# Kernel optimization log

Hardware: AMD Instinct MI355X
Metric: run time of the kernel (lower is better)

The kernel has to match this reference:

```python
import jax, jax.numpy as jnp
import numpy as np

N = 32768      # nodes
E = 524288     # edges (avg degree 16)
F = 64         # node_feat_dim
D = 64         # gnn_dim (= per-head out channels, concat=False)
ED = 32        # edge_feat_dim
L = 6          # num_layers
H = 2          # heads
C = D          # per-head channels
LN_EPS = 1e-5


def layer_norm(h, g, b):
    mu = jnp.mean(h, axis=-1, keepdims=True)
    var = jnp.mean((h - mu) ** 2, axis=-1, keepdims=True)
    return g * (h - mu) * jax.lax.rsqrt(var + LN_EPS) + b


def setup_inputs() -> dict:
    key = jax.random.key(0)
    ks = jax.random.split(key, 16)
    x = jax.random.normal(ks[0], (N, F), jnp.float32)
    edge_index = jax.random.randint(ks[1], (2, E), 0, N, jnp.int32)
    edge_attr = jax.random.normal(ks[2], (E, ED), jnp.float32)
    manual_gamma = 1.0 + 0.1 * jax.random.normal(ks[3], (L, D), jnp.float32)
    manual_beta = 0.1 * jax.random.normal(ks[4], (L, D), jnp.float32)
    # node_embed Linear(F, D)
    embed_W = jax.random.normal(ks[5], (F, D), jnp.float32) / np.float32(np.sqrt(F))
    embed_b = jnp.zeros((D,), jnp.float32)
    # per-layer LayerNorm affine params
    ln_gamma = jnp.ones((L, D), jnp.float32)
    ln_beta = jnp.zeros((L, D), jnp.float32)
    # per-layer GATConv params (shared lin for src/dst, PyG non-bipartite)
    lin_W = jax.random.normal(ks[6], (L, D, H * C), jnp.float32) / np.float32(np.sqrt(D))
    lin_edge_W = jax.random.normal(ks[7], (L, ED, H * C), jnp.float32) / np.float32(np.sqrt(ED))
    att_src = jax.random.normal(ks[8], (L, H, C), jnp.float32) / np.float32(np.sqrt(C))
    att_dst = jax.random.normal(ks[9], (L, H, C), jnp.float32) / np.float32(np.sqrt(C))
    att_edge = jax.random.normal(ks[10], (L, H, C), jnp.float32) / np.float32(np.sqrt(C))
    gat_bias = jnp.zeros((L, C), jnp.float32)
    # edge output head: Linear(2D+ED, D) -> ReLU -> Linear(D, 1)
    head_W1 = jax.random.normal(ks[11], (2 * D + ED, D), jnp.float32) / np.float32(np.sqrt(2 * D + ED))
    head_b1 = jnp.zeros((D,), jnp.float32)
    head_W2 = jax.random.normal(ks[12], (D, 1), jnp.float32) / np.float32(np.sqrt(D))
    head_b2 = jnp.zeros((1,), jnp.float32)
    return dict(x=x, edge_index=edge_index, edge_attr=edge_attr,
                manual_gamma=manual_gamma, manual_beta=manual_beta,
                embed_W=embed_W, embed_b=embed_b, ln_gamma=ln_gamma, ln_beta=ln_beta,
                lin_W=lin_W, lin_edge_W=lin_edge_W, att_src=att_src, att_dst=att_dst,
                att_edge=att_edge, gat_bias=gat_bias, head_W1=head_W1, head_b1=head_b1,
                head_W2=head_W2, head_b2=head_b2)


def reference(x, edge_index, edge_attr, manual_gamma, manual_beta,
              embed_W, embed_b, ln_gamma, ln_beta, lin_W, lin_edge_W,
              att_src, att_dst, att_edge, gat_bias, head_W1, head_b1,
              head_W2, head_b2):
    src, dst = edge_index[0], edge_index[1]
    # PyG GATConv default add_self_loops=True, fill_value='mean' for edge_attr
    loop = jnp.arange(N, dtype=edge_index.dtype)
    src_f = jnp.concatenate([src, loop])   # [E+N]
    dst_f = jnp.concatenate([dst, loop])
    deg = jax.ops.segment_sum(jnp.ones((E,), x.dtype), dst, num_segments=N)
    loop_attr = jax.ops.segment_sum(edge_attr, dst, num_segments=N) / jnp.maximum(deg, 1.0)[:, None]
    edge_attr_f = jnp.concatenate([edge_attr, loop_attr], axis=0)  # [E+N, ED]

    h = x @ embed_W + embed_b  # [N, D]
    for l in range(L):
        hn = layer_norm(h, ln_gamma[l], ln_beta[l])
        hm = manual_gamma[l][None, :] * hn + manual_beta[l][None, :]
        xh = (hm @ lin_W[l]).reshape(N, H, C)                      # [N,H,C]
        a_s = jnp.sum(xh * att_src[l][None], axis=-1)              # [N,H]
        a_d = jnp.sum(xh * att_dst[l][None], axis=-1)              # [N,H]
        eh = (edge_attr_f @ lin_edge_W[l]).reshape(-1, H, C)       # [E+N,H,C]
        a_e = jnp.sum(eh * att_edge[l][None], axis=-1)             # [E+N,H]
        alpha = jax.nn.leaky_relu(a_s[src_f] + a_d[dst_f] + a_e, 0.2)
        amax = jax.ops.segment_max(alpha, dst_f, num_segments=N)   # every node has a self-loop
        ex = jnp.exp(alpha - amax[dst_f])
        den = jax.ops.segment_sum(ex, dst_f, num_segments=N)
        w = ex / (den[dst_f] + 1e-16)                              # segment softmax [E+N,H]
        msg = xh[src_f] * w[..., None]                             # [E+N,H,C]
        out = jax.ops.segment_sum(msg, dst_f, num_segments=N)      # [N,H,C]
        h = jax.nn.relu(jnp.mean(out, axis=1) + gat_bias[l])       # concat=False -> head mean

    ef = jnp.concatenate([h[src], h[dst], edge_attr], axis=-1)     # [E, 2D+ED]
    hid = jax.nn.relu(ef @ head_W1 + head_b1)
    return (hid @ head_W2 + head_b2)[:, 0]                         # [E]
```

## Files before the change

### kernel.cpp

```cpp
#include <hip/hip_runtime.h>
#include <hip/hip_bf16.h>
#include <math.h>

#define NN 32768
#define EE 524288
#define LL 6

typedef __attribute__((ext_vector_type(8))) short short8;
typedef __attribute__((ext_vector_type(4))) float floatx4;
typedef __attribute__((ext_vector_type(4))) float fx4;
typedef __attribute__((ext_vector_type(2))) float fx2;

union U16x8 { short8 v; unsigned short u[8]; };

__device__ __forceinline__ unsigned short f2bf(float x) {
    union { float f; unsigned int u; } v; v.f = x;
    unsigned int r = v.u + 0x7fffu + ((v.u >> 16) & 1u);
    return (unsigned short)(r >> 16);
}
__device__ __forceinline__ float bf2f(unsigned short h) {
    union { unsigned int u; float f; } v; v.u = (unsigned int)h << 16;
    return v.f;
}


__global__ void deg_kernel(const int* __restrict__ dst, int* __restrict__ deg) {
    int i = (blockIdx.x * 256 + threadIdx.x) * 4;
    int4 d = *(const int4*)(dst + i);
    atomicAdd(&deg[d.x], 1);
    atomicAdd(&deg[d.y], 1);
    atomicAdd(&deg[d.z], 1);
    atomicAdd(&deg[d.w], 1);
}

__global__ __launch_bounds__(1024) void scan_kernel(const int* __restrict__ deg,
                                                    int* __restrict__ row_ptr,
                                                    int* __restrict__ cnt) {
    __shared__ int bs[1024];
    int t = threadIdx.x;
    int base = t * 32;
    int loc[32];
    int s = 0;
#pragma unroll
    for (int i = 0; i < 32; ++i) { int v = deg[base + i]; loc[i] = s; s += v; }
    bs[t] = s;
    __syncthreads();
    for (int off = 1; off < 1024; off <<= 1) {
        int v = (t >= off) ? bs[t - off] : 0;
        __syncthreads();
        bs[t] += v;
        __syncthreads();
    }
    int pre = (t == 0) ? 0 : bs[t - 1];
#pragma unroll
    for (int i = 0; i < 32; ++i) { row_ptr[base + i] = pre + loc[i]; cnt[base + i] = 0; }
    if (t == 1023) row_ptr[NN] = bs[1023];
}

__global__ void fill_kernel(const int* __restrict__ src, const int* __restrict__ dst,
                            const int* __restrict__ row_ptr, int* __restrict__ cnt,
                            int2* __restrict__ sedge) {
    int e = blockIdx.x * 256 + threadIdx.x;
    if (e >= EE) return;
    int d = dst[e];
    int pos = row_ptr[d] + atomicAdd(&cnt[d], 1);
    sedge[pos] = make_int2(e, src[e]);
}

__global__ __launch_bounds__(256) void smallprep_kernel(
    const float* __restrict__ lin_W, const float* __restrict__ head_W1,
    const float* __restrict__ lin_edge_W, const float* __restrict__ att_edge,
    const float* __restrict__ att_src, const float* __restrict__ att_dst,
    unsigned short* __restrict__ gBhi, unsigned short* __restrict__ gBlo,
    unsigned short* __restrict__ aeBhi, unsigned short* __restrict__ aeBlo,
    float* __restrict__ vs, float* __restrict__ vvd,
    unsigned short* __restrict__ w1chi, unsigned short* __restrict__ w1clo,
    int* __restrict__ deg) {
    __shared__ float svb[384];
    int bb = blockIdx.x;
    int tid = threadIdx.x;
    if (bb < 7) {
        unsigned short* dh = gBhi + (size_t)bb * 128 * 64;
        unsigned short* dl = gBlo + (size_t)bb * 128 * 64;
        if (bb < 6) {
            int n2 = tid & 63, kh = tid >> 6;
            U16x8 hh[4], ll[4];
            for (int kk = 0; kk < 32; ++kk) {
                int j = kh * 32 + kk;
                int h = j >> 6, k = j & 63;
                float wv = 0.5f * lin_W[((size_t)bb * 64 + k) * 128 + h * 64 + n2];
                unsigned short h16 = f2bf(wv);
                hh[kk >> 3].u[kk & 7] = h16;
                ll[kk >> 3].u[kk & 7] = f2bf(wv - bf2f(h16));
            }
#pragma unroll
            for (int c = 0; c < 4; ++c) {
                int cg = kh * 4 + c;
                int off = n2 * 128 + ((cg ^ (n2 & 15)) << 3);
                *(short8*)(dh + off) = hh[c].v;
                *(short8*)(dl + off) = ll[c].v;
            }
        } else {
            int n = tid & 127, kh = tid >> 7;
            U16x8 hh[4], ll[4];
            for (int kk = 0; kk < 32; ++kk) {
                int k = kh * 32 + kk;
                float wv = (n < 64) ? head_W1[k * 64 + n] : head_W1[(64 + k) * 64 + (n - 64)];
                unsigned short h16 = f2bf(wv);
                hh[kk >> 3].u[kk & 7] = h16;
                ll[kk >> 3].u[kk & 7] = f2bf(wv - bf2f(h16));
            }
#pragma unroll
            for (int c = 0; c < 4; ++c) {
                int cg = kh * 4 + c;
                int off = n * 64 + ((cg ^ (n & 7)) << 3);
                *(short8*)(dh + off) = hh[c].v;
                *(short8*)(dl + off) = ll[c].v;
            }
        }
    } else if (bb == 7) {
        for (int t = tid; t < 384; t += 256) {
            int l = t / 64; int r = t & 63; int ed = r >> 1; int hh = r & 1;
            const float* w = lin_edge_W + l * 32 * 128 + ed * 128 + hh * 64;
            const float* a = att_edge + l * 128 + hh * 64;
            float s = 0.f;
#pragma unroll 8
            for (int c = 0; c < 64; ++c) s += w[c] * a[c];
            svb[t] = s;
        }
        int n = tid & 63, kc = tid >> 6;
#pragma unroll
        for (int j = 0; j < 8; ++j) {
            int k = kc * 8 + j;
            float wv = head_W1[(128 + k) * 64 + n];
            unsigned short h16 = f2bf(wv);
            w1chi[n * 32 + k] = h16;
            w1clo[n * 32 + k] = f2bf(wv - bf2f(h16));
        }
        __syncthreads();
        if (tid < 64) {
            int n2 = tid & 15, q = tid >> 4;
            U16x8 hi, lo;
#pragma unroll
            for (int i = 0; i < 8; ++i) {
                int k = q * 8 + i;
                float val = (n2 < 12) ? svb[(n2 >> 1) * 64 + k * 2 + (n2 & 1)] : 0.f;
                unsigned short h16 = f2bf(val);
                hi.u[i] = h16;
                lo.u[i] = f2bf(val - bf2f(h16));
            }
            *(short8*)(aeBhi + tid * 8) = hi.v;
            *(short8*)(aeBlo + tid * 8) = lo.v;
        }
    } else if (bb < 14) {
        int l = bb - 8;
        int sel = tid >> 7, idx = tid & 127;
        int h = idx >> 6, k = idx & 63;
        const float* att = (sel ? att_dst : att_src) + l * 128 + h * 64;
        const float* wr = lin_W + ((size_t)l * 64 + k) * 128 + h * 64;
        float s = 0.f;
#pragma unroll 8
        for (int c = 0; c < 64; ++c) s += wr[c] * att[c];
        (sel ? vvd : vs)[l * 128 + idx] = s;
    } else {
        int i = (bb - 14) * 1024 + tid * 4;
        *(int4*)(deg + i) = make_int4(0, 0, 0, 0);
    }
}

__global__ __launch_bounds__(256) void ae_csr_kernel(
    const float* __restrict__ edge_attr, const int2* __restrict__ sedge,
    const unsigned short* __restrict__ aeBhi, const unsigned short* __restrict__ aeBlo,
    float* __restrict__ aeF, int* __restrict__ srcc) {
    __shared__ float tr[4][64 * 13];
    int tid = threadIdx.x;
    int w = tid >> 6, lane = tid & 63;
    int p0 = blockIdx.x * 256 + w * 64;
    short8 bhi = *(const short8*)(aeBhi + lane * 8);
    short8 blo = *(const short8*)(aeBlo + lane * 8);
    int r = lane & 15, q = lane >> 4;
    float* trw = tr[w];
#pragma unroll
    for (int t = 0; t < 4; ++t) {
        int eg = sedge[p0 + t * 16 + r].x;
        const fx4* p = (const fx4*)(edge_attr + (size_t)eg * 32 + q * 8);
        fx4 f0 = p[0], f1 = p[1];
        float av[8] = {f0.x, f0.y, f0.z, f0.w, f1.x, f1.y, f1.z, f1.w};
        U16x8 hi, lo;
#pragma unroll
        for (int jj = 0; jj < 8; ++jj) {
            unsigned short h16 = f2bf(av[jj]);
            hi.u[jj] = h16;
            lo.u[jj] = f2bf(av[jj] - bf2f(h16));
        }
        floatx4 acc = {};
        acc = __builtin_amdgcn_mfma_f32_16x16x32_bf16(lo.v, bhi, acc, 0, 0, 0);
        acc = __builtin_amdgcn_mfma_f32_16x16x32_bf16(hi.v, blo, acc, 0, 0, 0);
        acc = __builtin_amdgcn_mfma_f32_16x16x32_bf16(hi.v, bhi, acc, 0, 0, 0);
        if (r < 12) {
#pragma unroll
            for (int rr = 0; rr < 4; ++rr)
                trw[(t * 16 + q * 4 + rr) * 13 + r] = acc[rr];
        }
    }
    int2 sl = sedge[p0 + lane];
    srcc[p0 + lane] = sl.y;
#pragma unroll
    for (int l = 0; l < LL; ++l) {
        fx2 rec;
        rec.x = trw[lane * 13 + l * 2];
        rec.y = trw[lane * 13 + l * 2 + 1];
        __builtin_nontemporal_store(rec, (fx2*)(aeF + ((size_t)l * EE + p0 + lane) * 2));
    }
}

__global__ __launch_bounds__(256) void embed_ln_kernel(
    const float* __restrict__ x, const float* __restrict__ W, const float* __restrict__ b,
    const float* __restrict__ ln_g, const float* __restrict__ ln_b,
    const float* __restrict__ mg, const float* __restrict__ mb,
    const float* __restrict__ vs0, const float* __restrict__ vd0,
    unsigned short* __restrict__ hm_bf, float* __restrict__ a_s, float* __restrict__ a_d) {
    __shared__ float xr[4][64];
    int w = threadIdx.x >> 6, j = threadIdx.x & 63;
    int n = blockIdx.x * 4 + w;
    xr[w][j] = x[(size_t)n * 64 + j];
    __syncthreads();
    float acc = b[j];
#pragma unroll 8
    for (int k = 0; k < 64; ++k) acc += xr[w][k] * W[k * 64 + j];
    float s = acc, sq = acc * acc;
    for (int off = 1; off < 64; off <<= 1) { s += __shfl_xor(s, off); sq += __shfl_xor(sq, off); }
    float mu = s * (1.f / 64.f);
    float var = sq * (1.f / 64.f) - mu * mu;
    float rs = rsqrtf(var + 1e-5f);
    float hm = mg[j] * (ln_g[j] * (acc - mu) * rs + ln_b[j]) + mb[j];
    hm_bf[(size_t)n * 64 + j] = f2bf(hm);
    float s0 = hm * vs0[j], s1 = hm * vs0[64 + j];
    float d0 = hm * vd0[j], d1 = hm * vd0[64 + j];
    for (int off = 1; off < 64; off <<= 1) {
        s0 += __shfl_xor(s0, off); s1 += __shfl_xor(s1, off);
        d0 += __shfl_xor(d0, off); d1 += __shfl_xor(d1, off);
    }
    if (j == 0) {
        a_s[n * 2] = s0; a_s[n * 2 + 1] = s1;
        a_d[n * 2] = d0; a_d[n * 2 + 1] = d1;
    }
}

__device__ __forceinline__ void fma8h(uint4 pv, float w, float* a) {
    unsigned int u[4] = {pv.x, pv.y, pv.z, pv.w};
#pragma unroll
    for (int q = 0; q < 4; ++q) {
        union { unsigned int x; float f; } lo, hi;
        lo.x = u[q] << 16; hi.x = u[q] & 0xffff0000u;
        a[2 * q]     += w * lo.f;
        a[2 * q + 1] += w * hi.f;
    }
}

__device__ __forceinline__ void agg_node(
    int n, int ch, int hh, int j, const uint4* hmv, const float2* as2,
    const float* ad_in, const float* aeLl, const int* srcc,
    const int* row_ptr, float* sg, U16x8& hb) {
    float2 adn = ((const float2*)ad_in)[n];
    float2 asn = as2[n];
    uint4 pvself = hmv[(size_t)n * 8 + ch];
    int beg = row_ptr[n], end = row_ptr[n + 1];
    int degn = end - beg;
    float acc[8] = {};
    float den = 0.f, aex = 0.f, aey = 0.f;
    for (int base = 0; base < degn; base += 64) {
        int cnt = degn - base; cnt = cnt > 64 ? 64 : cnt;
        int nchunk = (cnt + 15) >> 4;
        for (int it = 0; it < nchunk; ++it) {
            int s0 = it * 16;
            int rem = cnt - s0;
            float w0v = 0.f, w1v = 0.f;
            int sval = 0;
            if (j < rem) {
                int idx = beg + base + s0 + j;
                int sv = srcc[idx];
                fx2 ae = *(const fx2*)(aeLl + (size_t)idx * 2);
                float2 as = as2[sv];
                aex += ae.x; aey += ae.y;
                float al0 = as.x + adn.x + ae.x; al0 = al0 > 0.f ? al0 : 0.2f * al0;
                float al1 = as.y + adn.y + ae.y; al1 = al1 > 0.f ? al1 : 0.2f * al1;
                w0v = __expf(al0);
                w1v = __expf(al1);
                sval = sv;
            }
            float4 st;
            st.x = __int_as_float(sval); st.y = w0v; st.z = w1v; st.w = 0.f;
            *(float4*)(sg + (s0 + j) * 4) = st;
        }
        int c8 = (cnt + 7) & ~7;
        for (int s = 0; s < c8; s += 8) {
            float4 m[8];
#pragma unroll
            for (int u = 0; u < 8; ++u) m[u] = *(const float4*)(sg + (s + u) * 4);
            uint4 p[8];
#pragma unroll
            for (int u = 0; u < 8; ++u) p[u] = hmv[(size_t)__float_as_int(m[u].x) * 8 + ch];
#pragma unroll
            for (int u = 0; u < 8; ++u) {
                float b = hh ? m[u].z : m[u].y;
                den += b;
                fma8h(p[u], b, acc);
            }
        }
    }
#pragma unroll
    for (int m = 1; m < 16; m <<= 1) {
        aex += __shfl_xor(aex, m);
        aey += __shfl_xor(aey, m);
    }
    float invd = 1.f / fmaxf((float)degn, 1.f);
    float al0 = asn.x + adn.x + aex * invd; al0 = al0 > 0.f ? al0 : 0.2f * al0;
    float al1 = asn.y + adn.y + aey * invd; al1 = al1 > 0.f ? al1 : 0.2f * al1;
    float ws = hh ? __expf(al1) : __expf(al0);
    den += ws;
    fma8h(pvself, ws, acc);
    float inv = 1.f / (den + 1e-16f);
#pragma unroll
    for (int q = 0; q < 8; ++q) hb.u[q] = f2bf(acc[q] * inv);
}

__global__ __launch_bounds__(256) void fused_post(
    const unsigned short* __restrict__ hm_in, const float* __restrict__ as_in,
    const float* __restrict__ ad_in, const float* __restrict__ aeLl,
    const int* __restrict__ srcc, const int* __restrict__ row_ptr,
    const unsigned short* __restrict__ gBhi, const unsigned short* __restrict__ gBlo,
    const float* __restrict__ bias, const float* __restrict__ ln_g,
    const float* __restrict__ ln_b, const float* __restrict__ mg,
    const float* __restrict__ mb, const float* __restrict__ vsn,
    const float* __restrict__ vdn, unsigned short* __restrict__ hm_out,
    float* __restrict__ as_out, float* __restrict__ ad_out) {
    __shared__ char smem[49152];
    unsigned short* Ahi = (unsigned short*)smem;
    float* stgAll = (float*)(smem + 16384);
    unsigned short* Bhi = (unsigned short*)(smem + 16384);
    unsigned short* Blo = (unsigned short*)(smem + 32768);
    int tid = threadIdx.x;
    int w = tid >> 6, lane = tid & 63;
    int g = lane >> 4, j = lane & 15;
    int ch = j & 7, hh = j >> 3;
    const float2* as2 = (const float2*)as_in;
    const uint4* hmv = (const uint4*)hm_in;
    float* sg = stgAll + w * 1024 + g * 256;
    int nb = blockIdx.x * 64;

    for (int rr = 0; rr < 4; ++rr) {
        int m = w * 16 + rr * 4 + g;
        U16x8 hb;
        agg_node(nb + m, ch, hh, j, hmv, as2, ad_in, aeLl, srcc, row_ptr, sg, hb);
        int cg = hh * 8 + ch;
        *(short8*)(Ahi + m * 128 + ((cg ^ (m & 15)) << 3)) = hb.v;
    }
    __syncthreads();
    {
        const uint4* sh = (const uint4*)gBhi;
        const uint4* sl = (const uint4*)gBlo;
        for (int i = tid; i < 1024; i += 256) {
            ((uint4*)Bhi)[i] = sh[i];
            ((uint4*)Blo)[i] = sl[i];
        }
    }
    __syncthreads();

    int col = lane & 15, quad = lane >> 4;
    int m = w * 16 + col;
    floatx4 acc[4] = {};
#pragma unroll
    for (int s = 0; s < 4; ++s) {
        int ca = (quad + 4 * s) ^ col;
        short8 ahi = *(const short8*)(Ahi + m * 128 + ca * 8);
#pragma unroll
        for (int t = 0; t < 4; ++t) {
            int off = (t * 16 + col) * 128 + ca * 8;
            short8 bhi = *(const short8*)(Bhi + off);
            short8 blo = *(const short8*)(Blo + off);
            acc[t] = __builtin_amdgcn_mfma_f32_16x16x32_bf16(ahi, blo, acc[t], 0, 0, 0);
            acc[t] = __builtin_amdgcn_mfma_f32_16x16x32_bf16(ahi, bhi, acc[t], 0, 0, 0);
        }
    }
    int nodebase = nb + w * 16;
    float bv[4];
#pragma unroll
    for (int t = 0; t < 4; ++t) bv[t] = bias[t * 16 + col];
    float vsv[4], vsv1[4], vdv[4], vdv1[4], lg[4], lb[4], mgv[4], mbv[4];
#pragma unroll
    for (int t = 0; t < 4; ++t) {
        int c = t * 16 + col;
        vsv[t] = vsn[c]; vsv1[t] = vsn[64 + c];
        vdv[t] = vdn[c]; vdv1[t] = vdn[64 + c];
        lg[t] = ln_g[c]; lb[t] = ln_b[c];
        mgv[t] = mg[c]; mbv[t] = mb[c];
    }
#pragma unroll
    for (int r = 0; r < 4; ++r) {
        int node = nodebase + quad * 4 + r;
        float hv[4];
        float s = 0.f, sq = 0.f;
#pragma unroll
        for (int t = 0; t < 4; ++t) {
            float v = acc[t][r] + bv[t];
            v = v > 0.f ? v : 0.f;
            hv[t] = v;
            s += v; sq += v * v;
        }
        for (int off = 1; off < 16; off <<= 1) { s += __shfl_xor(s, off); sq += __shfl_xor(sq, off); }
        float mu = s * (1.f / 64.f);
        float var = sq * (1.f / 64.f) - mu * mu;
        float rs = rsqrtf(var + 1e-5f);
        float s0 = 0.f, s1 = 0.f, d0 = 0.f, d1 = 0.f;
#pragma unroll
        for (int t = 0; t < 4; ++t) {
            float hmval = mgv[t] * (lg[t] * (hv[t] - mu) * rs + lb[t]) + mbv[t];
            hm_out[(size_t)node * 64 + t * 16 + col] = f2bf(hmval);
            s0 += hmval * vsv[t]; s1 += hmval * vsv1[t];
            d0 += hmval * vdv[t]; d1 += hmval * vdv1[t];
        }
        for (int off = 1; off < 16; off <<= 1) {
            s0 += __shfl_xor(s0, off); s1 += __shfl_xor(s1, off);
            d0 += __shfl_xor(d0, off); d1 += __shfl_xor(d1, off);
        }
        if (col == 0) {
            as_out[node * 2] = s0; as_out[node * 2 + 1] = s1;
            ad_out[node * 2] = d0; ad_out[node * 2 + 1] = d1;
        }
    }
}

__global__ __launch_bounds__(256) void fused_uv(
    const unsigned short* __restrict__ hm_in, const float* __restrict__ as_in,
    const float* __restrict__ ad_in, const float* __restrict__ aeLl,
    const int* __restrict__ srcc, const int* __restrict__ row_ptr,
    const unsigned short* __restrict__ gB5hi, const unsigned short* __restrict__ gB5lo,
    const float* __restrict__ bias,
    const unsigned short* __restrict__ gB6hi, const unsigned short* __restrict__ gB6lo,
    unsigned short* __restrict__ uv) {
    __shared__ char smem[49152];
    unsigned short* Ahi  = (unsigned short*)smem;
    float* stgAll        = (float*)(smem + 16384);
    unsigned short* B5hi = (unsigned short*)(smem + 16384);
    unsigned short* B5lo = (unsigned short*)(smem + 32768);
    unsigned short* A2hi = (unsigned short*)smem;
    unsigned short* A2lo = (unsigned short*)(smem + 8192);
    unsigned short* B6hi = (unsigned short*)(smem + 16384);
    unsigned short* B6lo = (unsigned short*)(smem + 32768);
    int tid = threadIdx.x;
    int w = tid >> 6, lane = tid & 63;
    int g = lane >> 4, j = lane & 15;
    int ch = j & 7, hh = j >> 3;
    const float2* as2 = (const float2*)as_in;
    const uint4* hmv = (const uint4*)hm_in;
    float* sg = stgAll + w * 1024 + g * 256;
    int nb = blockIdx.x * 64;

    for (int rr = 0; rr < 4; ++rr) {
        int m = w * 16 + rr * 4 + g;
        U16x8 hb;
        agg_node(nb + m, ch, hh, j, hmv, as2, ad_in, aeLl, srcc, row_ptr, sg, hb);
        int cg = hh * 8 + ch;
        *(short8*)(Ahi + m * 128 + ((cg ^ (m & 15)) << 3)) = hb.v;
    }
    __syncthreads();
    {
        const uint4* sh = (const uint4*)gB5hi;
        const uint4* sl = (const uint4*)gB5lo;
        for (int i = tid; i < 1024; i += 256) {
            ((uint4*)B5hi)[i] = sh[i];
            ((uint4*)B5lo)[i] = sl[i];
        }
    }
    __syncthreads();

    int col = lane & 15, quad = lane >> 4;
    int m = w * 16 + col;
    floatx4 acc[4] = {};
#pragma unroll
    for (int s = 0; s < 4; ++s) {
        int ca = (quad + 4 * s) ^ col;
        short8 ahi = *(const short8*)(Ahi + m * 128 + ca * 8);
#pragma unroll
        for (int t = 0; t < 4; ++t) {
            int off = (t * 16 + col) * 128 + ca * 8;
            short8 bhi = *(const short8*)(B5hi + off);
            short8 blo = *(const short8*)(B5lo + off);
            acc[t] = __builtin_amdgcn_mfma_f32_16x16x32_bf16(ahi, blo, acc[t], 0, 0, 0);
            acc[t] = __builtin_amdgcn_mfma_f32_16x16x32_bf16(ahi, bhi, acc[t], 0, 0, 0);
        }
    }
    float bv[4];
#pragma unroll
    for (int t = 0; t < 4; ++t) bv[t] = bias[t * 16 + col];
    __syncthreads();
#pragma unroll
    for (int t = 0; t < 4; ++t) {
        int c = t * 16 + col;
        int cg = c >> 3, cr = c & 7;
#pragma unroll
        for (int r = 0; r < 4; ++r) {
            float v = acc[t][r] + bv[t];
            v = v > 0.f ? v : 0.f;
            int i = w * 16 + quad * 4 + r;
            int off = i * 64 + ((cg ^ (i & 7)) << 3) + cr;
            unsigned short hhv = f2bf(v);
            A2hi[off] = hhv;
            A2lo[off] = f2bf(v - bf2f(hhv));
        }
    }
    for (int i = tid; i < 1024; i += 256) {
        ((uint4*)B6hi)[i] = ((const uint4*)gB6hi)[i];
        ((uint4*)B6lo)[i] = ((const uint4*)gB6lo)[i];
    }
    __syncthreads();

    floatx4 acc2[8] = {};
#pragma unroll
    for (int s = 0; s < 2; ++s) {
        int ca = (quad + 4 * s) ^ (col & 7);
        short8 a2h = *(const short8*)(A2hi + m * 64 + ca * 8);
        short8 a2l = *(const short8*)(A2lo + m * 64 + ca * 8);
#pragma unroll
        for (int t = 0; t < 8; ++t) {
            int off = (t * 16 + col) * 64 + ca * 8;
            short8 bh = *(const short8*)(B6hi + off);
            short8 bl = *(const short8*)(B6lo + off);
            acc2[t] = __builtin_amdgcn_mfma_f32_16x16x32_bf16(a2l, bh, acc2[t], 0, 0, 0);
            acc2[t] = __builtin_amdgcn_mfma_f32_16x16x32_bf16(a2h, bl, acc2[t], 0, 0, 0);
            acc2[t] = __builtin_amdgcn_mfma_f32_16x16x32_bf16(a2h, bh, acc2[t], 0, 0, 0);
        }
    }
    int nodebase = nb + w * 16;
#pragma unroll
    for (int t = 0; t < 8; ++t)
#pragma unroll
        for (int r = 0; r < 4; ++r)
            uv[(size_t)(nodebase + quad * 4 + r) * 128 + t * 16 + col] = f2bf(acc2[t][r]);
}

__global__ __launch_bounds__(256) void head2_kernel(
    const unsigned short* __restrict__ uv, const int* __restrict__ src,
    const int* __restrict__ dst, const float* __restrict__ edge_attr,
    const unsigned short* __restrict__ w1chi, const unsigned short* __restrict__ w1clo,
    const float* __restrict__ b1, const float* __restrict__ W2,
    const float* __restrict__ b2, float* __restrict__ out) {
    __shared__ float g[64][68];
    __shared__ unsigned short Abf[64 * 40];
    __shared__ unsigned short Bh[64 * 40], Bl[64 * 40];
    __shared__ int sA[64], dA[64];
    int tid = threadIdx.x;
    int base = blockIdx.x * 64;
    if (tid < 64) sA[tid] = src[base + tid];
    else if (tid < 128) dA[tid - 64] = dst[base + tid - 64];
    {
        int n = tid >> 2, c = tid & 3;
        *(short8*)(Bh + n * 40 + c * 8) = *(const short8*)(w1chi + n * 32 + c * 8);
        *(short8*)(Bl + n * 40 + c * 8) = *(const short8*)(w1clo + n * 32 + c * 8);
    }
    {
        int e = tid >> 2, q = tid & 3;
        const fx4* p = (const fx4*)(edge_attr + (size_t)(base + e) * 32 + q * 8);
        fx4 f0 = __builtin_nontemporal_load(p);
        fx4 f1 = __builtin_nontemporal_load(p + 1);
        float av[8] = {f0.x, f0.y, f0.z, f0.w, f1.x, f1.y, f1.z, f1.w};
        U16x8 cv;
#pragma unroll
        for (int jj = 0; jj < 8; ++jj) cv.u[jj] = f2bf(av[jj]);
        *(short8*)(Abf + e * 40 + q * 8) = cv.v;
    }
    __syncthreads();
    {
        int e = tid >> 2, q = tid & 3;
        const uint4* su = (const uint4*)(uv + (size_t)sA[e] * 128);
        const uint4* dv = (const uint4*)(uv + (size_t)dA[e] * 128);
        uint4 U0 = su[2 * q], U1 = su[2 * q + 1];
        uint4 V0 = dv[8 + 2 * q], V1 = dv[9 + 2 * q];
        const float4* b1p = (const float4*)(b1 + q * 16);
        float bb[16];
#pragma unroll
        for (int jj = 0; jj < 4; ++jj) {
            float4 b4 = b1p[jj];
            bb[4 * jj] = b4.x; bb[4 * jj + 1] = b4.y; bb[4 * jj + 2] = b4.z; bb[4 * jj + 3] = b4.w;
        }
        unsigned int uw[8] = {U0.x, U0.y, U0.z, U0.w, U1.x, U1.y, U1.z, U1.w};
        unsigned int vw[8] = {V0.x, V0.y, V0.z, V0.w, V1.x, V1.y, V1.z, V1.w};
        float* gr = &g[e][q * 16];
#pragma unroll
        for (int jj = 0; jj < 8; ++jj) {
            gr[2 * jj] = bf2f((unsigned short)(uw[jj] & 0xffff)) +
                         bf2f((unsigned short)(vw[jj] & 0xffff)) + bb[2 * jj];
            gr[2 * jj + 1] = bf2f((unsigned short)(uw[jj] >> 16)) +
                             bf2f((unsigned short)(vw[jj] >> 16)) + bb[2 * jj + 1];
        }
    }
    __syncthreads();

    int lane = tid & 63, w = tid >> 6, col = lane & 15, quad = lane >> 4;
    short8 a = *(const short8*)(Abf + (w * 16 + col) * 40 + quad * 8);
    floatx4 acc[4] = {};
#pragma unroll
    for (int t = 0; t < 4; ++t) {
        int off = (t * 16 + col) * 40 + quad * 8;
        short8 bh = *(const short8*)(Bh + off);
        short8 bl = *(const short8*)(Bl + off);
        acc[t] = __builtin_amdgcn_mfma_f32_16x16x32_bf16(a, bl, acc[t], 0, 0, 0);
        acc[t] = __builtin_amdgcn_mfma_f32_16x16x32_bf16(a, bh, acc[t], 0, 0, 0);
    }
    float sv[4] = {0.f, 0.f, 0.f, 0.f};
#pragma unroll
    for (int t = 0; t < 4; ++t) {
        float w2v = W2[t * 16 + col];
#pragma unroll
        for (int r = 0; r < 4; ++r) {
            float hid = acc[t][r] + g[w * 16 + quad * 4 + r][t * 16 + col];
            hid = hid > 0.f ? hid : 0.f;
            sv[r] += hid * w2v;
        }
    }
    float b2v = b2[0];
#pragma unroll
    for (int r = 0; r < 4; ++r) {
        float v = sv[r];
        v += __shfl_xor(v, 1);
        v += __shfl_xor(v, 2);
        v += __shfl_xor(v, 4);
        v += __shfl_xor(v, 8);
        if (col == 0) out[base + w * 16 + quad * 4 + r] = v + b2v;
    }
}


extern "C" void kernel_launch(void* const* d_in, const int* in_sizes, int n_in,
                              void* d_out, int out_size, void* d_ws, size_t ws_size,
                              hipStream_t stream) {
    const float* x            = (const float*)d_in[0];
    const int*   edge_index   = (const int*)d_in[1];
    const float* edge_attr    = (const float*)d_in[2];
    const float* manual_gamma = (const float*)d_in[3];
    const float* manual_beta  = (const float*)d_in[4];
    const float* embed_W      = (const float*)d_in[5];
    const float* embed_b      = (const float*)d_in[6];
    const float* ln_gamma     = (const float*)d_in[7];
    const float* ln_beta      = (const float*)d_in[8];
    const float* lin_W        = (const float*)d_in[9];
    const float* lin_edge_W   = (const float*)d_in[10];
    const float* att_src      = (const float*)d_in[11];
    const float* att_dst      = (const float*)d_in[12];
    const float* att_edge     = (const float*)d_in[13];
    const float* gat_bias     = (const float*)d_in[14];
    const float* head_W1      = (const float*)d_in[15];
    const float* head_b1      = (const float*)d_in[16];
    const float* head_W2      = (const float*)d_in[17];
    const float* head_b2      = (const float*)d_in[18];
    float* out = (float*)d_out;

    const int* src = edge_index;
    const int* dst = edge_index + EE;

    char* ws = (char*)d_ws;
    size_t off = 0;
    auto alloc = [&](size_t bytes) {
        void* p = ws + off;
        off += (bytes + 255) & ~(size_t)255;
        return p;
    };
    int*   deg        = (int*)alloc(NN * 4);
    int*   row_ptr    = (int*)alloc((NN + 1) * 4);
    int*   cnt        = (int*)alloc(NN * 4);
    int2*  sedge      = (int2*)alloc((size_t)EE * 8);
    int*   srcc       = (int*)alloc((size_t)EE * 4);
    float* aeF        = (float*)alloc((size_t)LL * EE * 8);
    float* vs         = (float*)alloc(LL * 128 * 4);
    float* vvd        = (float*)alloc(LL * 128 * 4);
    float* asA        = (float*)alloc((size_t)NN * 2 * 4);
    float* asB        = (float*)alloc((size_t)NN * 2 * 4);
    float* adA        = (float*)alloc((size_t)NN * 2 * 4);
    float* adB        = (float*)alloc((size_t)NN * 2 * 4);
    unsigned short* hmA   = (unsigned short*)alloc((size_t)NN * 64 * 2);
    unsigned short* hmB   = (unsigned short*)alloc((size_t)NN * 64 * 2);
    unsigned short* uvbuf = (unsigned short*)alloc((size_t)NN * 128 * 2);
    unsigned short* gBhi  = (unsigned short*)alloc((size_t)7 * 128 * 64 * 2);
    unsigned short* gBlo  = (unsigned short*)alloc((size_t)7 * 128 * 64 * 2);
    unsigned short* w1chi = (unsigned short*)alloc(64 * 32 * 2);
    unsigned short* w1clo = (unsigned short*)alloc(64 * 32 * 2);
    unsigned short* aeBhi = (unsigned short*)alloc(64 * 8 * 2);
    unsigned short* aeBlo = (unsigned short*)alloc(64 * 8 * 2);
    if (off > ws_size) return;

    smallprep_kernel<<<46, 256, 0, stream>>>(lin_W, head_W1, lin_edge_W, att_edge,
                                             att_src, att_dst, gBhi, gBlo, aeBhi, aeBlo,
                                             vs, vvd, w1chi, w1clo, deg);
    deg_kernel<<<EE / 1024, 256, 0, stream>>>(dst, deg);
    scan_kernel<<<1, 1024, 0, stream>>>(deg, row_ptr, cnt);
    fill_kernel<<<EE / 256, 256, 0, stream>>>(src, dst, row_ptr, cnt, sedge);
    ae_csr_kernel<<<EE / 256, 256, 0, stream>>>(edge_attr, sedge, aeBhi, aeBlo, aeF, srcc);
    embed_ln_kernel<<<NN / 4, 256, 0, stream>>>(x, embed_W, embed_b, ln_gamma, ln_beta,
                                                manual_gamma, manual_beta, vs, vvd,
                                                hmA, asA, adA);

    for (int l = 0; l < LL; ++l) {
        const unsigned short* hin = (l & 1) ? hmB : hmA;
        unsigned short* hout = (l & 1) ? hmA : hmB;
        const float* asi = (l & 1) ? asB : asA;
        float* aso = (l & 1) ? asA : asB;
        const float* adi = (l & 1) ? adB : adA;
        float* ado = (l & 1) ? adA : adB;
        const float* aeLl = aeF + (size_t)l * EE * 2;
        if (l < LL - 1) {
            fused_post<<<NN / 64, 256, 0, stream>>>(
                hin, asi, adi, aeLl, srcc, row_ptr,
                gBhi + (size_t)l * 128 * 64, gBlo + (size_t)l * 128 * 64,
                gat_bias + l * 64, ln_gamma + (l + 1) * 64, ln_beta + (l + 1) * 64,
                manual_gamma + (l + 1) * 64, manual_beta + (l + 1) * 64,
                vs + (l + 1) * 128, vvd + (l + 1) * 128, hout, aso, ado);
        } else {
            fused_uv<<<NN / 64, 256, 0, stream>>>(
                hin, asi, adi, aeLl, srcc, row_ptr,
                gBhi + (size_t)l * 128 * 64, gBlo + (size_t)l * 128 * 64,
                gat_bias + l * 64, gBhi + (size_t)6 * 128 * 64,
                gBlo + (size_t)6 * 128 * 64, uvbuf);
        }
    }

    head2_kernel<<<EE / 64, 256, 0, stream>>>(uvbuf, src, dst, edge_attr, w1chi, w1clo,
                                              head_b1, head_W2, head_b2, out);
}
```

Baseline: 436.1 us.

## Process edge head in CSR order and halve nodes per GAT block

The edge-output head now walks edges in dst-sorted CSR order. It reads a bf16 copy of edge_attr written during the CSR pass and a stored dst array, and scatters each result back to its original edge index. This is meant to improve locality of the dst-row gathers in uv and to halve edge_attr read bytes in the head. Separately, the fused aggregation kernels now handle 32 nodes per block instead of 64, doubling the grid and shrinking LDS, with only two waves doing the MFMA/LN stage. The costs are an extra bf16 edge_attr write and a scattered output store.

New measurement: 490.3 us. 12.4% more time.

```diff
diff --git a/kernel.cpp b/kernel.cpp
--- a/kernel.cpp
+++ b/kernel.cpp
@@ -59,12 +59,13 @@
 
 __global__ void fill_kernel(const int* __restrict__ src, const int* __restrict__ dst,
                             const int* __restrict__ row_ptr, int* __restrict__ cnt,
-                            int2* __restrict__ sedge) {
+                            int2* __restrict__ sedge, int* __restrict__ dstc) {
     int e = blockIdx.x * 256 + threadIdx.x;
     if (e >= EE) return;
     int d = dst[e];
     int pos = row_ptr[d] + atomicAdd(&cnt[d], 1);
     sedge[pos] = make_int2(e, src[e]);
+    dstc[pos] = d;
 }
 
 __global__ __launch_bounds__(256) void smallprep_kernel(
@@ -171,7 +172,7 @@
 __global__ __launch_bounds__(256) void ae_csr_kernel(
     const float* __restrict__ edge_attr, const int2* __restrict__ sedge,
     const unsigned short* __restrict__ aeBhi, const unsigned short* __restrict__ aeBlo,
-    float* __restrict__ aeF, int* __restrict__ srcc) {
+    float* __restrict__ aeF, int* __restrict__ srcc, unsigned short* __restrict__ eabf) {
     __shared__ float tr[4][64 * 13];
     int tid = threadIdx.x;
     int w = tid >> 6, lane = tid & 63;
@@ -193,6 +194,7 @@
             hi.u[jj] = h16;
             lo.u[jj] = f2bf(av[jj] - bf2f(h16));
         }
+        __builtin_nontemporal_store(hi.v, (short8*)(eabf + (size_t)(p0 + t * 16 + r) * 32 + q * 8));
         floatx4 acc = {};
         acc = __builtin_amdgcn_mfma_f32_16x16x32_bf16(lo.v, bhi, acc, 0, 0, 0);
         acc = __builtin_amdgcn_mfma_f32_16x16x32_bf16(hi.v, blo, acc, 0, 0, 0);
@@ -335,11 +337,11 @@
     const float* __restrict__ mb, const float* __restrict__ vsn,
     const float* __restrict__ vdn, unsigned short* __restrict__ hm_out,
     float* __restrict__ as_out, float* __restrict__ ad_out) {
-    __shared__ char smem[49152];
+    __shared__ char smem[40960];
     unsigned short* Ahi = (unsigned short*)smem;
-    float* stgAll = (float*)(smem + 16384);
-    unsigned short* Bhi = (unsigned short*)(smem + 16384);
-    unsigned short* Blo = (unsigned short*)(smem + 32768);
+    float* stgAll = (float*)(smem + 8192);
+    unsigned short* Bhi = (unsigned short*)(smem + 8192);
+    unsigned short* Blo = (unsigned short*)(smem + 24576);
     int tid = threadIdx.x;
     int w = tid >> 6, lane = tid & 63;
     int g = lane >> 4, j = lane & 15;
@@ -347,10 +349,10 @@
     const float2* as2 = (const float2*)as_in;
     const uint4* hmv = (const uint4*)hm_in;
     float* sg = stgAll + w * 1024 + g * 256;
-    int nb = blockIdx.x * 64;
-
-    for (int rr = 0; rr < 4; ++rr) {
-        int m = w * 16 + rr * 4 + g;
+    int nb = blockIdx.x * 32;
+
+    for (int rr = 0; rr < 2; ++rr) {
+        int m = w * 8 + rr * 4 + g;
         U16x8 hb;
         agg_node(nb + m, ch, hh, j, hmv, as2, ad_in, aeLl, srcc, row_ptr, sg, hb);
         int cg = hh * 8 + ch;
@@ -367,66 +369,68 @@
     }
     __syncthreads();
 
-    int col = lane & 15, quad = lane >> 4;
-    int m = w * 16 + col;
-    floatx4 acc[4] = {};
-#pragma unroll
-    for (int s = 0; s < 4; ++s) {
-        int ca = (quad + 4 * s) ^ col;
-        short8 ahi = *(const short8*)(Ahi + m * 128 + ca * 8);
+    if (w < 2) {
+        int col = lane & 15, quad = lane >> 4;
+        int m = w * 16 + col;
+        floatx4 acc[4] = {};
+#pragma unroll
+        for (int s = 0; s < 4; ++s) {
+            int ca = (quad + 4 * s) ^ col;
+            short8 ahi = *(const short8*)(Ahi + m * 128 + ca * 8);
+#pragma unroll
+            for (int t = 0; t < 4; ++t) {
+                int off = (t * 16 + col) * 128 + ca * 8;
+                short8 bhi = *(const short8*)(Bhi + off);
+                short8 blo = *(const short8*)(Blo + off);
+                acc[t] = __builtin_amdgcn_mfma_f32_16x16x32_bf16(ahi, blo, acc[t], 0, 0, 0);
+                acc[t] = __builtin_amdgcn_mfma_f32_16x16x32_bf16(ahi, bhi, acc[t], 0, 0, 0);
+            }
+        }
+        int nodebase = nb + w * 16;
+        float bv[4];
+#pragma unroll
+        for (int t = 0; t < 4; ++t) bv[t] = bias[t * 16 + col];
+        float vsv[4], vsv1[4], vdv[4], vdv1[4], lg[4], lb[4], mgv[4], mbv[4];
 #pragma unroll
         for (int t = 0; t < 4; ++t) {
-            int off = (t * 16 + col) * 128 + ca * 8;
-            short8 bhi = *(const short8*)(Bhi + off);
-            short8 blo = *(const short8*)(Blo + off);
-            acc[t] = __builtin_amdgcn_mfma_f32_16x16x32_bf16(ahi, blo, acc[t], 0, 0, 0);
-            acc[t] = __builtin_amdgcn_mfma_f32_16x16x32_bf16(ahi, bhi, acc[t], 0, 0, 0);
-        }
-    }
-    int nodebase = nb + w * 16;
-    float bv[4];
-#pragma unroll
-    for (int t = 0; t < 4; ++t) bv[t] = bias[t * 16 + col];
-    float vsv[4], vsv1[4], vdv[4], vdv1[4], lg[4], lb[4], mgv[4], mbv[4];
-#pragma unroll
-    for (int t = 0; t < 4; ++t) {
-        int c = t * 16 + col;
-        vsv[t] = vsn[c]; vsv1[t] = vsn[64 + c];
-        vdv[t] = vdn[c]; vdv1[t] = vdn[64 + c];
-        lg[t] = ln_g[c]; lb[t] = ln_b[c];
-        mgv[t] = mg[c]; mbv[t] = mb[c];
-    }
-#pragma unroll
-    for (int r = 0; r < 4; ++r) {
-        int node = nodebase + quad * 4 + r;
-        float hv[4];
-        float s = 0.f, sq = 0.f;
-#pragma unroll
-        for (int t = 0; t < 4; ++t) {
-            float v = acc[t][r] + bv[t];
-            v = v > 0.f ? v : 0.f;
-            hv[t] = v;
-            s += v; sq += v * v;
-        }
-        for (int off = 1; off < 16; off <<= 1) { s += __shfl_xor(s, off); sq += __shfl_xor(sq, off); }
-        float mu = s * (1.f / 64.f);
-        float var = sq * (1.f / 64.f) - mu * mu;
-        float rs = rsqrtf(var + 1e-5f);
-        float s0 = 0.f, s1 = 0.f, d0 = 0.f, d1 = 0.f;
-#pragma unroll
-        for (int t = 0; t < 4; ++t) {
-            float hmval = mgv[t] * (lg[t] * (hv[t] - mu) * rs + lb[t]) + mbv[t];
-            hm_out[(size_t)node * 64 + t * 16 + col] = f2bf(hmval);
-            s0 += hmval * vsv[t]; s1 += hmval * vsv1[t];
-            d0 += hmval * vdv[t]; d1 += hmval * vdv1[t];
-        }
-        for (int off = 1; off < 16; off <<= 1) {
-            s0 += __shfl_xor(s0, off); s1 += __shfl_xor(s1, off);
-            d0 += __shfl_xor(d0, off); d1 += __shfl_xor(d1, off);
-        }
-        if (col == 0) {
-            as_out[node * 2] = s0; as_out[node * 2 + 1] = s1;
-            ad_out[node * 2] = d0; ad_out[node * 2 + 1] = d1;
+            int c = t * 16 + col;
+            vsv[t] = vsn[c]; vsv1[t] = vsn[64 + c];
+            vdv[t] = vdn[c]; vdv1[t] = vdn[64 + c];
+            lg[t] = ln_g[c]; lb[t] = ln_b[c];
+            mgv[t] = mg[c]; mbv[t] = mb[c];
+        }
+#pragma unroll
+        for (int r = 0; r < 4; ++r) {
+            int node = nodebase + quad * 4 + r;
+            float hv[4];
+            float s = 0.f, sq = 0.f;
+#pragma unroll
+            for (int t = 0; t < 4; ++t) {
+                float v = acc[t][r] + bv[t];
+                v = v > 0.f ? v : 0.f;
+                hv[t] = v;
+                s += v; sq += v * v;
+            }
+            for (int off = 1; off < 16; off <<= 1) { s += __shfl_xor(s, off); sq += __shfl_xor(sq, off); }
+            float mu = s * (1.f / 64.f);
+            float var = sq * (1.f / 64.f) - mu * mu;
+            float rs = rsqrtf(var + 1e-5f);
+            float s0 = 0.f, s1 = 0.f, d0 = 0.f, d1 = 0.f;
+#pragma unroll
+            for (int t = 0; t < 4; ++t) {
+                float hmval = mgv[t] * (lg[t] * (hv[t] - mu) * rs + lb[t]) + mbv[t];
+                hm_out[(size_t)node * 64 + t * 16 + col] = f2bf(hmval);
+                s0 += hmval * vsv[t]; s1 += hmval * vsv1[t];
+                d0 += hmval * vdv[t]; d1 += hmval * vdv1[t];
+            }
+            for (int off = 1; off < 16; off <<= 1) {
+                s0 += __shfl_xor(s0, off); s1 += __shfl_xor(s1, off);
+                d0 += __shfl_xor(d0, off); d1 += __shfl_xor(d1, off);
+            }
+            if (col == 0) {
+                as_out[node * 2] = s0; as_out[node * 2 + 1] = s1;
+                ad_out[node * 2] = d0; ad_out[node * 2 + 1] = d1;
+            }
         }
     }
 }
@@ -439,15 +443,15 @@
     const float* __restrict__ bias,
     const unsigned short* __restrict__ gB6hi, const unsigned short* __restrict__ gB6lo,
     unsigned short* __restrict__ uv) {
-    __shared__ char smem[49152];
+    __shared__ char smem[40960];
     unsigned short* Ahi  = (unsigned short*)smem;
-    float* stgAll        = (float*)(smem + 16384);
-    unsigned short* B5hi = (unsigned short*)(smem + 16384);
-    unsigned short* B5lo = (unsigned short*)(smem + 32768);
+    float* stgAll        = (float*)(smem + 8192);
+    unsigned short* B5hi = (unsigned short*)(smem + 8192);
+    unsigned short* B5lo = (unsigned short*)(smem + 24576);
     unsigned short* A2hi = (unsigned short*)smem;
-    unsigned short* A2lo = (unsigned short*)(smem + 8192);
-    unsigned short* B6hi = (unsigned short*)(smem + 16384);
-    unsigned short* B6lo = (unsigned short*)(smem + 32768);
+    unsigned short* A2lo = (unsigned short*)(smem + 4096);
+    unsigned short* B6hi = (unsigned short*)(smem + 8192);
+    unsigned short* B6lo = (unsigned short*)(smem + 24576);
     int tid = threadIdx.x;
     int w = tid >> 6, lane = tid & 63;
     int g = lane >> 4, j = lane & 15;
@@ -455,10 +459,10 @@
     const float2* as2 = (const float2*)as_in;
     const uint4* hmv = (const uint4*)hm_in;
     float* sg = stgAll + w * 1024 + g * 256;
-    int nb = blockIdx.x * 64;
-
-    for (int rr = 0; rr < 4; ++rr) {
-        int m = w * 16 + rr * 4 + g;
+    int nb = blockIdx.x * 32;
+
+    for (int rr = 0; rr < 2; ++rr) {
+        int m = w * 8 + rr * 4 + g;
         U16x8 hb;
         agg_node(nb + m, ch, hh, j, hmv, as2, ad_in, aeLl, srcc, row_ptr, sg, hb);
         int cg = hh * 8 + ch;
@@ -478,36 +482,40 @@
     int col = lane & 15, quad = lane >> 4;
     int m = w * 16 + col;
     floatx4 acc[4] = {};
-#pragma unroll
-    for (int s = 0; s < 4; ++s) {
-        int ca = (quad + 4 * s) ^ col;
-        short8 ahi = *(const short8*)(Ahi + m * 128 + ca * 8);
+    if (w < 2) {
+#pragma unroll
+        for (int s = 0; s < 4; ++s) {
+            int ca = (quad + 4 * s) ^ col;
+            short8 ahi = *(const short8*)(Ahi + m * 128 + ca * 8);
+#pragma unroll
+            for (int t = 0; t < 4; ++t) {
+                int off = (t * 16 + col) * 128 + ca * 8;
+                short8 bhi = *(const short8*)(B5hi + off);
+                short8 blo = *(const short8*)(B5lo + off);
+                acc[t] = __builtin_amdgcn_mfma_f32_16x16x32_bf16(ahi, blo, acc[t], 0, 0, 0);
+                acc[t] = __builtin_amdgcn_mfma_f32_16x16x32_bf16(ahi, bhi, acc[t], 0, 0, 0);
+            }
+        }
+    }
+    __syncthreads();
+    if (w < 2) {
+        float bv[4];
+#pragma unroll
+        for (int t = 0; t < 4; ++t) bv[t] = bias[t * 16 + col];
 #pragma unroll
         for (int t = 0; t < 4; ++t) {
-            int off = (t * 16 + col) * 128 + ca * 8;
-            short8 bhi = *(const short8*)(B5hi + off);
-            short8 blo = *(const short8*)(B5lo + off);
-            acc[t] = __builtin_amdgcn_mfma_f32_16x16x32_bf16(ahi, blo, acc[t], 0, 0, 0);
-            acc[t] = __builtin_amdgcn_mfma_f32_16x16x32_bf16(ahi, bhi, acc[t], 0, 0, 0);
-        }
-    }
-    float bv[4];
-#pragma unroll
-    for (int t = 0; t < 4; ++t) bv[t] = bias[t * 16 + col];
-    __syncthreads();
-#pragma unroll
-    for (int t = 0; t < 4; ++t) {
-        int c = t * 16 + col;
-        int cg = c >> 3, cr = c & 7;
-#pragma unroll
-        for (int r = 0; r < 4; ++r) {
-            float v = acc[t][r] + bv[t];
-            v = v > 0.f ? v : 0.f;
-            int i = w * 16 + quad * 4 + r;
-            int off = i * 64 + ((cg ^ (i & 7)) << 3) + cr;
-            unsigned short hhv = f2bf(v);
-            A2hi[off] = hhv;
-            A2lo[off] = f2bf(v - bf2f(hhv));
+            int c = t * 16 + col;
+            int cg = c >> 3, cr = c & 7;
+#pragma unroll
+            for (int r = 0; r < 4; ++r) {
+                float v = acc[t][r] + bv[t];
+                v = v > 0.f ? v : 0.f;
+                int i = w * 16 + quad * 4 + r;
+                int off = i * 64 + ((cg ^ (i & 7)) << 3) + cr;
+                unsigned short hhv = f2bf(v);
+                A2hi[off] = hhv;
+                A2lo[off] = f2bf(v - bf2f(hhv));
+            }
         }
     }
     for (int i = tid; i < 1024; i += 256) {
@@ -516,44 +524,51 @@
     }
     __syncthreads();
 
-    floatx4 acc2[8] = {};
-#pragma unroll
-    for (int s = 0; s < 2; ++s) {
-        int ca = (quad + 4 * s) ^ (col & 7);
-        short8 a2h = *(const short8*)(A2hi + m * 64 + ca * 8);
-        short8 a2l = *(const short8*)(A2lo + m * 64 + ca * 8);
-#pragma unroll
-        for (int t = 0; t < 8; ++t) {
-            int off = (t * 16 + col) * 64 + ca * 8;
-            short8 bh = *(const short8*)(B6hi + off);
-            short8 bl = *(const short8*)(B6lo + off);
-            acc2[t] = __builtin_amdgcn_mfma_f32_16x16x32_bf16(a2l, bh, acc2[t], 0, 0, 0);
-            acc2[t] = __builtin_amdgcn_mfma_f32_16x16x32_bf16(a2h, bl, acc2[t], 0, 0, 0);
-            acc2[t] = __builtin_amdgcn_mfma_f32_16x16x32_bf16(a2h, bh, acc2[t], 0, 0, 0);
-        }
-    }
-    int nodebase = nb + w * 16;
-#pragma unroll
-    for (int t = 0; t < 8; ++t)
-#pragma unroll
-        for (int r = 0; r < 4; ++r)
-            uv[(size_t)(nodebase + quad * 4 + r) * 128 + t * 16 + col] = f2bf(acc2[t][r]);
+    if (w < 2) {
+        floatx4 acc2[8] = {};
+#pragma unroll
+        for (int s = 0; s < 2; ++s) {
+            int ca = (quad + 4 * s) ^ (col & 7);
+            short8 a2h = *(const short8*)(A2hi + m * 64 + ca * 8);
+            short8 a2l = *(const short8*)(A2lo + m * 64 + ca * 8);
+#pragma unroll
+            for (int t = 0; t < 8; ++t) {
+                int off = (t * 16 + col) * 64 + ca * 8;
+                short8 bh = *(const short8*)(B6hi + off);
+                short8 bl = *(const short8*)(B6lo + off);
+                acc2[t] = __builtin_amdgcn_mfma_f32_16x16x32_bf16(a2l, bh, acc2[t], 0, 0, 0);
+                acc2[t] = __builtin_amdgcn_mfma_f32_16x16x32_bf16(a2h, bl, acc2[t], 0, 0, 0);
+                acc2[t] = __builtin_amdgcn_mfma_f32_16x16x32_bf16(a2h, bh, acc2[t], 0, 0, 0);
+            }
+        }
+        int nodebase = nb + w * 16;
+#pragma unroll
+        for (int t = 0; t < 8; ++t)
+#pragma unroll
+            for (int r = 0; r < 4; ++r)
+                uv[(size_t)(nodebase + quad * 4 + r) * 128 + t * 16 + col] = f2bf(acc2[t][r]);
+    }
 }
 
 __global__ __launch_bounds__(256) void head2_kernel(
-    const unsigned short* __restrict__ uv, const int* __restrict__ src,
-    const int* __restrict__ dst, const float* __restrict__ edge_attr,
+    const unsigned short* __restrict__ uv, const int2* __restrict__ sedge,
+    const int* __restrict__ dstc, const unsigned short* __restrict__ eabf,
     const unsigned short* __restrict__ w1chi, const unsigned short* __restrict__ w1clo,
     const float* __restrict__ b1, const float* __restrict__ W2,
     const float* __restrict__ b2, float* __restrict__ out) {
     __shared__ float g[64][68];
     __shared__ unsigned short Abf[64 * 40];
     __shared__ unsigned short Bh[64 * 40], Bl[64 * 40];
-    __shared__ int sA[64], dA[64];
+    __shared__ int sA[64], dA[64], eidA[64];
     int tid = threadIdx.x;
     int base = blockIdx.x * 64;
-    if (tid < 64) sA[tid] = src[base + tid];
-    else if (tid < 128) dA[tid - 64] = dst[base + tid - 64];
+    if (tid < 64) {
+        int2 se = sedge[base + tid];
+        eidA[tid] = se.x;
+        sA[tid] = se.y;
+    } else if (tid < 128) {
+        dA[tid - 64] = dstc[base + tid - 64];
+    }
     {
         int n = tid >> 2, c = tid & 3;
         *(short8*)(Bh + n * 40 + c * 8) = *(const short8*)(w1chi + n * 32 + c * 8);
@@ -561,14 +576,9 @@
     }
     {
         int e = tid >> 2, q = tid & 3;
-        const fx4* p = (const fx4*)(edge_attr + (size_t)(base + e) * 32 + q * 8);
-        fx4 f0 = __builtin_nontemporal_load(p);
-        fx4 f1 = __builtin_nontemporal_load(p + 1);
-        float av[8] = {f0.x, f0.y, f0.z, f0.w, f1.x, f1.y, f1.z, f1.w};
-        U16x8 cv;
-#pragma unroll
-        for (int jj = 0; jj < 8; ++jj) cv.u[jj] = f2bf(av[jj]);
-        *(short8*)(Abf + e * 40 + q * 8) = cv.v;
+        short8 v = __builtin_nontemporal_load(
+            (const short8*)(eabf + (size_t)(base + e) * 32 + q * 8));
+        *(short8*)(Abf + e * 40 + q * 8) = v;
     }
     __syncthreads();
     {
@@ -627,7 +637,7 @@
         v += __shfl_xor(v, 2);
         v += __shfl_xor(v, 4);
         v += __shfl_xor(v, 8);
-        if (col == 0) out[base + w * 16 + quad * 4 + r] = v + b2v;
+        if (col == 0) out[eidA[w * 16 + quad * 4 + r]] = v + b2v;
     }
 }
 
@@ -671,7 +681,9 @@
     int*   cnt        = (int*)alloc(NN * 4);
     int2*  sedge      = (int2*)alloc((size_t)EE * 8);
     int*   srcc       = (int*)alloc((size_t)EE * 4);
+    int*   dstc       = (int*)alloc((size_t)EE * 4);
     float* aeF        = (float*)alloc((size_t)LL * EE * 8);
+    unsigned short* eabf = (unsigned short*)alloc((size_t)EE * 32 * 2);
     float* vs         = (float*)alloc(LL * 128 * 4);
     float* vvd        = (float*)alloc(LL * 128 * 4);
     float* asA        = (float*)alloc((size_t)NN * 2 * 4);
@@ -694,8 +706,9 @@
                                              vs, vvd, w1chi, w1clo, deg);
     deg_kernel<<<EE / 1024, 256, 0, stream>>>(dst, deg);
     scan_kernel<<<1, 1024, 0, stream>>>(deg, row_ptr, cnt);
-    fill_kernel<<<EE / 256, 256, 0, stream>>>(src, dst, row_ptr, cnt, sedge);
-    ae_csr_kernel<<<EE / 256, 256, 0, stream>>>(edge_attr, sedge, aeBhi, aeBlo, aeF, srcc);
+    fill_kernel<<<EE / 256, 256, 0, stream>>>(src, dst, row_ptr, cnt, sedge, dstc);
+    ae_csr_kernel<<<EE / 256, 256, 0, stream>>>(edge_attr, sedge, aeBhi, aeBlo,
+                                                aeF, srcc, eabf);
     embed_ln_kernel<<<NN / 4, 256, 0, stream>>>(x, embed_W, embed_b, ln_gamma, ln_beta,
                                                 manual_gamma, manual_beta, vs, vvd,
                                                 hmA, asA, adA);
@@ -709,14 +722,14 @@
         float* ado = (l & 1) ? adA : adB;
         const float* aeLl = aeF + (size_t)l * EE * 2;
         if (l < LL - 1) {
-            fused_post<<<NN / 64, 256, 0, stream>>>(
+            fused_post<<<NN / 32, 256, 0, stream>>>(
                 hin, asi, adi, aeLl, srcc, row_ptr,
                 gBhi + (size_t)l * 128 * 64, gBlo + (size_t)l * 128 * 64,
                 gat_bias + l * 64, ln_gamma + (l + 1) * 64, ln_beta + (l + 1) * 64,
                 manual_gamma + (l + 1) * 64, manual_beta + (l + 1) * 64,
                 vs + (l + 1) * 128, vvd + (l + 1) * 128, hout, aso, ado);
         } else {
-            fused_uv<<<NN / 64, 256, 0, stream>>>(
+            fused_uv<<<NN / 32, 256, 0, stream>>>(
                 hin, asi, adi, aeLl, srcc, row_ptr,
                 gBhi + (size_t)l * 128 * 64, gBlo + (size_t)l * 128 * 64,
                 gat_bias + l * 64, gBhi + (size_t)6 * 128 * 64,
@@ -724,6 +737,6 @@
         }
     }
 
-    head2_kernel<<<EE / 64, 256, 0, stream>>>(uvbuf, src, dst, edge_attr, w1chi, w1clo,
+    head2_kernel<<<EE / 64, 256, 0, stream>>>(uvbuf, sedge, dstc, eabf, w1chi, w1clo,
                                               head_b1, head_W2, head_b2, out);
 }
```
